# Kernel optimization log

Measured on AMD Instinct MI355X. Metric: run time of the kernel, lower is better.

Reference implementation:

```python
import jax, jax.numpy as jnp
import numpy as np

B, M, K = 32768, 8192, 16
EPS = 1e-5  # torch BatchNorm1d default


def _bn_relu(x, g, b):
    # training-mode batch norm (biased variance), matching torch BatchNorm1d forward
    m = x.mean(0)
    v = x.var(0)
    return jax.nn.relu(g * (x - m) * jax.lax.rsqrt(v + EPS) + b)


def _forward(pos, mc, mv, w1, b1, w2, b2, w3, b3, w4, b4, w5, b5, w6, b6,
             g1, be1, g2, be2, g3, be3, g4, be4, g5, be5, k):
    # squared pairwise distances [B, M]; same ordering as L2 norm used by torch.sort
    d2 = (pos * pos).sum(1, keepdims=True) + (mc * mc).sum(1)[None, :] - 2.0 * (pos @ mc.T)
    _, idx = jax.lax.top_k(-d2, k)                     # k nearest indices [B, k]
    nb = jnp.concatenate([mc[idx], mv[idx]], axis=-1)  # [B, k, 4] = (coord, value) per neighbor
    knn_feat = jnp.concatenate([pos, nb.reshape(pos.shape[0], k * 4)], axis=1)  # [B, 2+4k]
    x = _bn_relu(knn_feat @ w1 + b1, g1, be1)
    x = _bn_relu(x @ w2 + b2, g2, be2)
    x = _bn_relu(x @ w3 + b3, g3, be3)
    x = _bn_relu(x @ w4 + b4, g4, be4)
    x = _bn_relu(x @ w5 + b5, g5, be5)  # dropout = identity (eval mode)
    x = x @ w6 + b6
    return x, knn_feat


def setup_inputs() -> dict:
    key = jax.random.key(0)
    ks = jax.random.split(key, 32)
    d_in = 2 + K * 4
    dims = [(d_in, 128), (128, 256), (256, 512), (512, 128), (128, 64), (64, 2)]
    inp = {
        "pos": jax.random.normal(ks[0], (B, 2), jnp.float32),
        "measure_coords": jax.random.normal(ks[1], (M, 2), jnp.float32),
        "measure_vals": jax.random.normal(ks[2], (M, 2), jnp.float32),
    }
    for i, (fi, fo) in enumerate(dims, 1):
        inp[f"w{i}"] = jax.random.normal(ks[2 + 2 * i], (fi, fo), jnp.float32) / np.float32(np.sqrt(fi))
        inp[f"b{i}"] = jnp.zeros((fo,), jnp.float32)
    for i, n in enumerate([128, 256, 512, 128, 64], 1):
        inp[f"g{i}"] = jnp.ones((n,), jnp.float32)
        inp[f"be{i}"] = jnp.zeros((n,), jnp.float32)
    inp["k"] = K
    return inp


def reference(pos, measure_coords, measure_vals, w1, b1, w2, b2, w3, b3, w4, b4,
              w5, b5, w6, b6, g1, be1, g2, be2, g3, be3, g4, be4, g5, be5, k):
    return _forward(pos, measure_coords, measure_vals, w1, b1, w2, b2, w3, b3, w4,
                    b4, w5, b5, w6, b6, g1, be1, g2, be2, g3, be3, g4, be4, g5, be5, k)
```

## Files before the change

kernel.cpp:

```cpp
#include <hip/hip_runtime.h>

typedef unsigned short u16;
typedef unsigned int   u32;
typedef __attribute__((ext_vector_type(8))) short bf16x8;
typedef __attribute__((ext_vector_type(4))) float f32x4;

#define B_ROWS 32768
#define EPS_BN 1e-5f

__device__ __forceinline__ u16 f2bf(float f) {
  u32 u = __float_as_uint(f);
  u32 r = (u + 0x7FFFu + ((u >> 16) & 1u)) >> 16;
  return (u16)r;
}
__device__ __forceinline__ float bf2f(u16 h) {
  return __uint_as_float(((u32)h) << 16);
}

__device__ __forceinline__ float dcalc(float px, float py, float sp, float mx, float my) {
#pragma clang fp contract(off)
  float sm   = mx * mx + my * my;
  float pm   = px * mx;
  float dot  = __builtin_fmaf(py, my, pm);
  float spsm = sp + sm;
  return spsm - 2.0f * dot;
}
__device__ __forceinline__ float dcalc2(float px, float py, float sp, float mx, float my,
                                        float sm) {
#pragma clang fp contract(off)
  float pm   = px * mx;
  float dot  = __builtin_fmaf(py, my, pm);
  float spsm = sp + sm;
  return spsm - 2.0f * dot;
}
__device__ __forceinline__ float smcalc(float mx, float my) {
#pragma clang fp contract(off)
  return mx * mx + my * my;
}
__device__ __forceinline__ float spcalc(float px, float py) {
#pragma clang fp contract(off)
  return px * px + py * py;
}
#define MED3 __builtin_amdgcn_fmed3f

__global__ __launch_bounds__(256, 4)
void knn_kernel(const float2* __restrict__ pos, const float2* __restrict__ mc,
                const float2* __restrict__ mv, float* __restrict__ knn_out,
                u16* __restrict__ X0)
{
  __shared__ float tv[32 * 130];
  __shared__ float tstS[32];
  __shared__ int   qcnt[32];

  const int t = threadIdx.x;
  const int g = t >> 6;
  const int s = t & 63;
  const int q0 = blockIdx.x * 32;

  float px[8], py[8], sp[8];
#pragma unroll
  for (int j = 0; j < 8; ++j) {
    float2 p = pos[q0 + g * 8 + j];
    px[j] = p.x; py[j] = p.y; sp[j] = spcalc(p.x, p.y);
  }

  const float4* mc4 = (const float4*)mc;
  const int b4 = s * 64;
  const int basePt = s * 128;

  float z0[8], z1[8];
#pragma unroll
  for (int j = 0; j < 8; ++j) { z0[j] = __builtin_inff(); z1[j] = __builtin_inff(); }

  float4 cur = mc4[b4];
  for (int i = 0; i < 64; ++i) {
    float4 nxt = mc4[b4 + ((i + 1) & 63)];
    float smA = smcalc(cur.x, cur.y);
    float smB = smcalc(cur.z, cur.w);
#pragma unroll
    for (int j = 0; j < 8; ++j) {
      float dA = dcalc2(px[j], py[j], sp[j], cur.x, cur.y, smA);
      z1[j] = MED3(z0[j], dA, z1[j]); z0[j] = fminf(z0[j], dA);
      float dB = dcalc2(px[j], py[j], sp[j], cur.z, cur.w, smB);
      z1[j] = MED3(z0[j], dB, z1[j]); z0[j] = fminf(z0[j], dB);
    }
    cur = nxt;
  }
#pragma unroll
  for (int j = 0; j < 8; ++j) {
    tv[(g * 8 + j) * 130 + s * 2 + 0] = z0[j];
    tv[(g * 8 + j) * 130 + s * 2 + 1] = z1[j];
  }
  __syncthreads();

  if (t < 32) {
    float ch[16];
#pragma unroll
    for (int j = 0; j < 16; ++j) ch[j] = __builtin_inff();
    for (int k = 0; k < 128; ++k) {
      float v = tv[t * 130 + k];
#pragma unroll
      for (int j = 15; j >= 1; --j) ch[j] = MED3(ch[j-1], v, ch[j]);
      ch[0] = fminf(ch[0], v);
    }
    tstS[t] = ch[15];
    qcnt[t] = 0;
  }
  __syncthreads();
  float Tq[8];
#pragma unroll
  for (int j = 0; j < 8; ++j) Tq[j] = tstS[g * 8 + j];
  __syncthreads();

  u16* qcand = (u16*)tv;
  for (int i = 0; i < 64; ++i) {
    float4 c2 = mc4[b4 + i];
    float smA = smcalc(c2.x, c2.y);
    float smB = smcalc(c2.z, c2.w);
    const int idxA = basePt + 2 * i;
#pragma unroll
    for (int j = 0; j < 8; ++j) {
      float dA = dcalc2(px[j], py[j], sp[j], c2.x, c2.y, smA);
      if (dA <= Tq[j]) {
        int o = atomicAdd(&qcnt[g * 8 + j], 1);
        if (o < 64) qcand[(g * 8 + j) * 64 + o] = (u16)idxA;
      }
      float dB = dcalc2(px[j], py[j], sp[j], c2.z, c2.w, smB);
      if (dB <= Tq[j]) {
        int o = atomicAdd(&qcnt[g * 8 + j], 1);
        if (o < 64) qcand[(g * 8 + j) * 64 + o] = (u16)(idxA + 1);
      }
    }
  }
  __syncthreads();

  if (t < 32) {
    const int q = q0 + t;
    float2 p = pos[q];
    const float sq = spcalc(p.x, p.y);
    int cnt = qcnt[t]; if (cnt > 64) cnt = 64;
    float fd[16]; int fi[16];
#pragma unroll
    for (int j = 0; j < 16; ++j) { fd[j] = __builtin_inff(); fi[j] = 0x7fffffff; }
    for (int j = 0; j < cnt; ++j) {
      int ci = qcand[t * 64 + j];
      float2 m = mc[ci];
      float d = dcalc(p.x, p.y, sq, m.x, m.y);
      bool cc = (d < fd[15]) || (d == fd[15] && ci < fi[15]);
      if (cc) {
#pragma unroll
        for (int k = 15; k >= 1; --k) {
          bool cm = (d < fd[k-1]) || (d == fd[k-1] && ci < fi[k-1]);
          if (cc) {
            if (cm) { fd[k] = fd[k-1]; fi[k] = fi[k-1]; }
            else    { fd[k] = d;       fi[k] = ci;      }
          }
          cc = cm;
        }
        if (cc) { fd[0] = d; fi[0] = ci; }
      }
    }
    float* orow = knn_out + (size_t)q * 66;
    u16*   xrow = X0 + (size_t)q * 96;
    orow[0] = p.x; orow[1] = p.y;
    xrow[0] = f2bf(p.x); xrow[1] = f2bf(p.y);
#pragma unroll
    for (int j = 0; j < 16; ++j) {
      int ci = fi[j];
      float2 m = mc[ci], v = mv[ci];
      orow[2 + 4*j + 0] = m.x; orow[2 + 4*j + 1] = m.y;
      orow[2 + 4*j + 2] = v.x; orow[2 + 4*j + 3] = v.y;
      xrow[2 + 4*j + 0] = f2bf(m.x); xrow[2 + 4*j + 1] = f2bf(m.y);
      xrow[2 + 4*j + 2] = f2bf(v.x); xrow[2 + 4*j + 3] = f2bf(v.y);
    }
#pragma unroll
    for (int c = 66; c < 96; ++c) xrow[c] = 0;
  }
}

__global__ __launch_bounds__(256)
void prep_wt_all(const float* __restrict__ w1, const float* __restrict__ w2,
                 const float* __restrict__ w3, const float* __restrict__ w4,
                 const float* __restrict__ w5,
                 u16* __restrict__ wt1, u16* __restrict__ wt2, u16* __restrict__ wt3,
                 u16* __restrict__ wt4, u16* __restrict__ wt5)
{
  const int l = blockIdx.y;
  const float* w; u16* wt; int K, N, Kp;
  if (l == 0)      { w = w1; wt = wt1; K = 66;  N = 128; Kp = 96;  }
  else if (l == 1) { w = w2; wt = wt2; K = 128; N = 256; Kp = 128; }
  else if (l == 2) { w = w3; wt = wt3; K = 256; N = 512; Kp = 256; }
  else if (l == 3) { w = w4; wt = wt4; K = 512; N = 128; Kp = 512; }
  else             { w = w5; wt = wt5; K = 128; N = 64;  Kp = 128; }
  int i = blockIdx.x * 256 + threadIdx.x;
  if (i >= N * Kp) return;
  int n = i / Kp, kp = i - n * Kp;
  float v = (kp < K) ? w[(size_t)kp * N + n] : 0.0f;
  wt[i] = f2bf(v);
}

template<int BN, bool FUSE>
__global__ __launch_bounds__(256)
void gemm_bn_kernel(const u16* __restrict__ X, int Kw,
                    const u16* __restrict__ WT,
                    const float* __restrict__ bias,
                    const float* __restrict__ psum, const float* __restrict__ psq,
                    const float* __restrict__ gw,   const float* __restrict__ bw,
                    u16* __restrict__ Z, int N,
                    float* __restrict__ csum, float* __restrict__ csq)
{
  constexpr int BM = 128;
  constexpr int AST = 40;
  __shared__ u16 Ash[BM * AST];
  __shared__ u16 Bsh[BN * AST];
  __shared__ float redS[4][BN];
  __shared__ float redQ[4][BN];
  __shared__ float scA[512];
  __shared__ float ttA[512];

  const int t = threadIdx.x;
  const int wave = t >> 6;
  const int lane = t & 63;
  const int lr = lane & 15;
  const int qd = lane >> 4;
  const int m0 = blockIdx.x * BM;
  const int n0 = blockIdx.y * BN;

  if (FUSE) {
    const float invB = 1.0f / 32768.0f;
    for (int c = t; c < Kw; c += 256) {
      float mean = psum[c] * invB;
      float var  = __fmaf_rn(-mean, mean, psq[c] * invB);
      float sc   = gw[c] * rsqrtf(var + EPS_BN);
      scA[c] = sc;
      ttA[c] = __fmaf_rn(-mean, sc, bw[c]);
    }
    __syncthreads();
  }

  f32x4 acc[2][BN / 16];
#pragma unroll
  for (int a = 0; a < 2; ++a)
#pragma unroll
    for (int b = 0; b < BN / 16; ++b) {
      acc[a][b][0] = 0.f; acc[a][b][1] = 0.f; acc[a][b][2] = 0.f; acc[a][b][3] = 0.f;
    }

  const int sr = t >> 2;
  const int sk = (t & 3) * 8;

  for (int k0 = 0; k0 < Kw; k0 += 32) {
#pragma unroll
    for (int rr = 0; rr < 2; ++rr) {
      int r = sr + rr * 64;
      uint4 g = *(const uint4*)(&X[(size_t)(m0 + r) * Kw + k0 + sk]);
      if (FUSE) {
        u32 w[4] = {g.x, g.y, g.z, g.w};
        u32 o[4];
#pragma unroll
        for (int e = 0; e < 4; ++e) {
          int kk = k0 + sk + 2 * e;
          float lo = bf2f((u16)(w[e] & 0xffffu));
          float hi = bf2f((u16)(w[e] >> 16));
          float yl = fmaxf(__fmaf_rn(lo, scA[kk],     ttA[kk]),     0.0f);
          float yh = fmaxf(__fmaf_rn(hi, scA[kk + 1], ttA[kk + 1]), 0.0f);
          o[e] = (u32)f2bf(yl) | ((u32)f2bf(yh) << 16);
        }
        g.x = o[0]; g.y = o[1]; g.z = o[2]; g.w = o[3];
      }
      *(uint4*)(&Ash[r * AST + sk]) = g;
    }
    if (BN == 128) {
#pragma unroll
      for (int rr = 0; rr < 2; ++rr) {
        int n = sr + rr * 64;
        *(uint4*)(&Bsh[n * AST + sk]) =
            *(const uint4*)(&WT[(size_t)(n0 + n) * Kw + k0 + sk]);
      }
    } else {
      int n = sr;
      *(uint4*)(&Bsh[n * AST + sk]) =
          *(const uint4*)(&WT[(size_t)(n0 + n) * Kw + k0 + sk]);
    }
    __syncthreads();
    bf16x8 af0 = *(const bf16x8*)(&Ash[(wave * 32 + lr) * AST + qd * 8]);
    bf16x8 af1 = *(const bf16x8*)(&Ash[(wave * 32 + 16 + lr) * AST + qd * 8]);
#pragma unroll
    for (int ct = 0; ct < BN / 16; ++ct) {
      bf16x8 bfr = *(const bf16x8*)(&Bsh[(ct * 16 + lr) * AST + qd * 8]);
      acc[0][ct] = __builtin_amdgcn_mfma_f32_16x16x32_bf16(af0, bfr, acc[0][ct], 0, 0, 0);
      acc[1][ct] = __builtin_amdgcn_mfma_f32_16x16x32_bf16(af1, bfr, acc[1][ct], 0, 0, 0);
    }
    __syncthreads();
  }

#pragma unroll
  for (int ct = 0; ct < BN / 16; ++ct) {
    int cg = n0 + ct * 16 + lr;
    float bv = bias[cg];
    float s = 0.f, sqv = 0.f;
#pragma unroll
    for (int rt = 0; rt < 2; ++rt) {
#pragma unroll
      for (int r = 0; r < 4; ++r) {
        float z = acc[rt][ct][r] + bv;
        int row = m0 + wave * 32 + rt * 16 + qd * 4 + r;
        Z[(size_t)row * N + cg] = f2bf(z);
        s += z;
        sqv = __fmaf_rn(z, z, sqv);
      }
    }
    s   += __shfl_xor(s, 16);   s   += __shfl_xor(s, 32);
    sqv += __shfl_xor(sqv, 16); sqv += __shfl_xor(sqv, 32);
    if (qd == 0) { redS[wave][ct * 16 + lr] = s; redQ[wave][ct * 16 + lr] = sqv; }
  }
  __syncthreads();
  if (t < BN) {
    float s  = redS[0][t] + redS[1][t] + redS[2][t] + redS[3][t];
    float sv = redQ[0][t] + redQ[1][t] + redQ[2][t] + redQ[3][t];
    atomicAdd(&csum[n0 + t], s);
    atomicAdd(&csq[n0 + t], sv);
  }
}

__global__ __launch_bounds__(256)
void gemv6_kernel(const u16* __restrict__ Z5, const float* __restrict__ w6,
                  const float* __restrict__ b6,
                  const float* __restrict__ psum, const float* __restrict__ psq,
                  const float* __restrict__ gw,   const float* __restrict__ bw,
                  float* __restrict__ out)
{
  __shared__ float wsh[128];
  __shared__ float scs[64];
  __shared__ float tts[64];
  const int t = threadIdx.x;
  if (t < 128) wsh[t] = w6[t];
  if (t < 64) {
    const float invB = 1.0f / 32768.0f;
    float mean = psum[t] * invB;
    float var  = __fmaf_rn(-mean, mean, psq[t] * invB);
    float sc   = gw[t] * rsqrtf(var + EPS_BN);
    scs[t] = sc;
    tts[t] = __fmaf_rn(-mean, sc, bw[t]);
  }
  __syncthreads();
  const int q = blockIdx.x * 256 + t;
  const uint4* xv = (const uint4*)(Z5 + (size_t)q * 64);
  float a0 = 0.f, a1 = 0.f;
#pragma unroll
  for (int cc = 0; cc < 8; ++cc) {
    uint4 pk = xv[cc];
    u32 u[4] = {pk.x, pk.y, pk.z, pk.w};
#pragma unroll
    for (int uu = 0; uu < 4; ++uu) {
      int k = cc * 8 + uu * 2;
      float z0 = bf2f((u16)(u[uu] & 0xffffu));
      float z1 = bf2f((u16)(u[uu] >> 16));
      float x0 = fmaxf(__fmaf_rn(z0, scs[k],     tts[k]),     0.0f);
      float x1 = fmaxf(__fmaf_rn(z1, scs[k + 1], tts[k + 1]), 0.0f);
      x0 = bf2f(f2bf(x0));
      x1 = bf2f(f2bf(x1));
      a0 = __fmaf_rn(x0, wsh[2 * k + 0], a0);
      a1 = __fmaf_rn(x0, wsh[2 * k + 1], a1);
      a0 = __fmaf_rn(x1, wsh[2 * k + 2], a0);
      a1 = __fmaf_rn(x1, wsh[2 * k + 3], a1);
    }
  }
  float2 o; o.x = a0 + b6[0]; o.y = a1 + b6[1];
  ((float2*)out)[q] = o;
}

extern "C" void kernel_launch(void* const* d_in, const int* in_sizes, int n_in,
                              void* d_out, int out_size, void* d_ws, size_t ws_size,
                              hipStream_t stream)
{
  const float2* pos = (const float2*)d_in[0];
  const float2* mc  = (const float2*)d_in[1];
  const float2* mv  = (const float2*)d_in[2];
  const float* w1 = (const float*)d_in[3];  const float* b1 = (const float*)d_in[4];
  const float* w2 = (const float*)d_in[5];  const float* b2 = (const float*)d_in[6];
  const float* w3 = (const float*)d_in[7];  const float* b3 = (const float*)d_in[8];
  const float* w4 = (const float*)d_in[9];  const float* b4 = (const float*)d_in[10];
  const float* w5 = (const float*)d_in[11]; const float* b5 = (const float*)d_in[12];
  const float* w6 = (const float*)d_in[13]; const float* b6 = (const float*)d_in[14];
  const float* g1 = (const float*)d_in[15]; const float* be1 = (const float*)d_in[16];
  const float* g2 = (const float*)d_in[17]; const float* be2 = (const float*)d_in[18];
  const float* g3 = (const float*)d_in[19]; const float* be3 = (const float*)d_in[20];
  const float* g4 = (const float*)d_in[21]; const float* be4 = (const float*)d_in[22];
  const float* g5 = (const float*)d_in[23]; const float* be5 = (const float*)d_in[24];

  char* ws = (char*)d_ws;
  u16* X0   = (u16*)(ws + 0);
  u16* ZA   = (u16*)(ws + 6291456);
  u16* ZB   = (u16*)(ws + 39845888);
  u16* WT1  = (u16*)(ws + 73400320);
  u16* WT2  = (u16*)(ws + 73424896);
  u16* WT3  = (u16*)(ws + 73490432);
  u16* WT4  = (u16*)(ws + 73752576);
  u16* WT5  = (u16*)(ws + 73883648);
  float* stats = (float*)(ws + 73900032);
  float* s1 = stats;        float* s2 = stats + 128;  float* s3 = stats + 384;
  float* s4 = stats + 896;  float* s5 = stats + 1024;
  float* sqb = stats + 1088;
  float* q1 = sqb;          float* q2 = sqb + 128;    float* q3 = sqb + 384;
  float* q4 = sqb + 896;    float* q5 = sqb + 1024;

  float* outX = (float*)d_out;
  float* outK = outX + 2 * B_ROWS;

  hipMemsetAsync(stats, 0, 2176 * sizeof(float), stream);
  prep_wt_all<<<dim3(512, 5), 256, 0, stream>>>(w1, w2, w3, w4, w5, WT1, WT2, WT3, WT4, WT5);
  knn_kernel<<<dim3(1024), 256, 0, stream>>>(pos, mc, mv, outK, X0);

  gemm_bn_kernel<64, false><<<dim3(256, 2), 256, 0, stream>>>(
      X0, 96, WT1, b1, nullptr, nullptr, nullptr, nullptr, ZA, 128, s1, q1);
  gemm_bn_kernel<64, true><<<dim3(256, 4), 256, 0, stream>>>(
      ZA, 128, WT2, b2, s1, q1, g1, be1, ZB, 256, s2, q2);
  gemm_bn_kernel<64, true><<<dim3(256, 8), 256, 0, stream>>>(
      ZB, 256, WT3, b3, s2, q2, g2, be2, ZA, 512, s3, q3);
  gemm_bn_kernel<64, true><<<dim3(256, 2), 256, 0, stream>>>(
      ZA, 512, WT4, b4, s3, q3, g3, be3, ZB, 128, s4, q4);
  gemm_bn_kernel<64, true><<<dim3(256, 1), 256, 0, stream>>>(
      ZB, 128, WT5, b5, s4, q4, g4, be4, ZA, 64, s5, q5);
  gemv6_kernel<<<dim3(128), 256, 0, stream>>>(ZA, w6, b6, s5, q5, g5, be5, outX);

  (void)in_sizes; (void)n_in; (void)out_size; (void)ws_size;
}
```

Before: 358.6 us.

## Fuse MLP stages into one persistent kernel with software grid barriers

Replaces the weight-prep kernel, the five GEMM+BN launches and the final GEMV with a single persistent kernel of 512 blocks that moves between phases through a sense-reversal grid barrier. The BN+ReLU normalisation is no longer fused into the next GEMM's A-load; it becomes a separate in-place apply pass over each activation buffer. The two wider GEMMs switch to 128-column tiles. This removes launch overhead and the repeated per-tile BN recomputation, but adds extra full read/write passes over the activations and relies on all 512 blocks being co-resident, which is not guaranteed and can deadlock otherwise.

```diff
diff --git a/kernel.cpp b/kernel.cpp
--- a/kernel.cpp
+++ b/kernel.cpp
@@ -178,161 +178,198 @@
   }
 }
 
-__global__ __launch_bounds__(256)
-void prep_wt_all(const float* __restrict__ w1, const float* __restrict__ w2,
-                 const float* __restrict__ w3, const float* __restrict__ w4,
-                 const float* __restrict__ w5,
-                 u16* __restrict__ wt1, u16* __restrict__ wt2, u16* __restrict__ wt3,
-                 u16* __restrict__ wt4, u16* __restrict__ wt5)
-{
-  const int l = blockIdx.y;
-  const float* w; u16* wt; int K, N, Kp;
-  if (l == 0)      { w = w1; wt = wt1; K = 66;  N = 128; Kp = 96;  }
-  else if (l == 1) { w = w2; wt = wt2; K = 128; N = 256; Kp = 128; }
-  else if (l == 2) { w = w3; wt = wt3; K = 256; N = 512; Kp = 256; }
-  else if (l == 3) { w = w4; wt = wt4; K = 512; N = 128; Kp = 512; }
-  else             { w = w5; wt = wt5; K = 128; N = 64;  Kp = 128; }
-  int i = blockIdx.x * 256 + threadIdx.x;
-  if (i >= N * Kp) return;
-  int n = i / Kp, kp = i - n * Kp;
-  float v = (kp < K) ? w[(size_t)kp * N + n] : 0.0f;
-  wt[i] = f2bf(v);
-}
-
-template<int BN, bool FUSE>
-__global__ __launch_bounds__(256)
-void gemm_bn_kernel(const u16* __restrict__ X, int Kw,
-                    const u16* __restrict__ WT,
-                    const float* __restrict__ bias,
-                    const float* __restrict__ psum, const float* __restrict__ psq,
-                    const float* __restrict__ gw,   const float* __restrict__ bw,
-                    u16* __restrict__ Z, int N,
-                    float* __restrict__ csum, float* __restrict__ csq)
-{
-  constexpr int BM = 128;
+struct MlpArgs {
+  const u16* X0;
+  u16 *ZA, *ZB;
+  u16 *WT1, *WT2, *WT3, *WT4, *WT5;
+  const float *w1,*b1,*w2,*b2,*w3,*b3,*w4,*b4,*w5,*b5,*w6,*b6;
+  const float *g1,*be1,*g2,*be2,*g3,*be3,*g4,*be4,*g5,*be5;
+  float* stats;
+  int*   bar;
+  float* outX;
+};
+
+#define MLP_GRID 512
+
+__device__ __forceinline__ void grid_barrier(int* bar, int& sense)
+{
+  __syncthreads();
+  if (threadIdx.x == 0) {
+    ++sense;
+    __threadfence();
+    if (atomicAdd(&bar[0], 1) == MLP_GRID - 1) {
+      atomicExch(&bar[0], 0);
+      __threadfence();
+      atomicExch(&bar[1], sense);
+    } else {
+      while (atomicAdd(&bar[1], 0) < sense) { __builtin_amdgcn_s_sleep(2); }
+    }
+    __threadfence();
+  }
+  __syncthreads();
+}
+
+__device__ void prep_phase(const MlpArgs& a)
+{
+  const int gid  = blockIdx.x * 256 + threadIdx.x;
+  const int nthr = MLP_GRID * 256;
+  if (gid < 2176) a.stats[gid] = 0.0f;
+  for (int i = gid; i < 249856; i += nthr) {
+    int r = i; const float* w; u16* wt; int N, K, Kp;
+    if (r < 12288)                 { w = a.w1; wt = a.WT1; N = 128; K = 66;  Kp = 96;  }
+    else if ((r -= 12288) < 32768) { w = a.w2; wt = a.WT2; N = 256; K = 128; Kp = 128; }
+    else if ((r -= 32768) < 131072){ w = a.w3; wt = a.WT3; N = 512; K = 256; Kp = 256; }
+    else if ((r -= 131072) < 65536){ w = a.w4; wt = a.WT4; N = 128; K = 512; Kp = 512; }
+    else { r -= 65536;               w = a.w5; wt = a.WT5; N = 64;  K = 128; Kp = 128; }
+    int n = r / Kp, kp = r - n * Kp;
+    float v = (kp < K) ? w[(size_t)kp * N + n] : 0.0f;
+    wt[r] = f2bf(v);
+  }
+}
+
+template<int BN>
+__device__ void gemm_phase(const u16* __restrict__ X, int Kw,
+                           const u16* __restrict__ WT, const float* __restrict__ bias,
+                           u16* __restrict__ Z, int N,
+                           float* csum, float* csq, char* smem)
+{
   constexpr int AST = 40;
-  __shared__ u16 Ash[BM * AST];
-  __shared__ u16 Bsh[BN * AST];
-  __shared__ float redS[4][BN];
-  __shared__ float redQ[4][BN];
-  __shared__ float scA[512];
-  __shared__ float ttA[512];
+  u16*   Ash  = (u16*)smem;
+  u16*   Bsh  = (u16*)(smem + 10240);
+  float* redS = (float*)(smem + 20480);
+  float* redQ = (float*)(smem + 22528);
 
   const int t = threadIdx.x;
   const int wave = t >> 6;
   const int lane = t & 63;
   const int lr = lane & 15;
   const int qd = lane >> 4;
-  const int m0 = blockIdx.x * BM;
-  const int n0 = blockIdx.y * BN;
-
-  if (FUSE) {
-    const float invB = 1.0f / 32768.0f;
-    for (int c = t; c < Kw; c += 256) {
-      float mean = psum[c] * invB;
-      float var  = __fmaf_rn(-mean, mean, psq[c] * invB);
-      float sc   = gw[c] * rsqrtf(var + EPS_BN);
-      scA[c] = sc;
-      ttA[c] = __fmaf_rn(-mean, sc, bw[c]);
-    }
-    __syncthreads();
-  }
-
-  f32x4 acc[2][BN / 16];
-#pragma unroll
-  for (int a = 0; a < 2; ++a)
-#pragma unroll
-    for (int b = 0; b < BN / 16; ++b) {
-      acc[a][b][0] = 0.f; acc[a][b][1] = 0.f; acc[a][b][2] = 0.f; acc[a][b][3] = 0.f;
-    }
-
   const int sr = t >> 2;
   const int sk = (t & 3) * 8;
 
-  for (int k0 = 0; k0 < Kw; k0 += 32) {
-#pragma unroll
-    for (int rr = 0; rr < 2; ++rr) {
-      int r = sr + rr * 64;
-      uint4 g = *(const uint4*)(&X[(size_t)(m0 + r) * Kw + k0 + sk]);
-      if (FUSE) {
-        u32 w[4] = {g.x, g.y, g.z, g.w};
-        u32 o[4];
-#pragma unroll
-        for (int e = 0; e < 4; ++e) {
-          int kk = k0 + sk + 2 * e;
-          float lo = bf2f((u16)(w[e] & 0xffffu));
-          float hi = bf2f((u16)(w[e] >> 16));
-          float yl = fmaxf(__fmaf_rn(lo, scA[kk],     ttA[kk]),     0.0f);
-          float yh = fmaxf(__fmaf_rn(hi, scA[kk + 1], ttA[kk + 1]), 0.0f);
-          o[e] = (u32)f2bf(yl) | ((u32)f2bf(yh) << 16);
+  const int nTiles = 256 * (N / BN);
+  for (int tile = blockIdx.x; tile < nTiles; tile += MLP_GRID) {
+    const int m0 = (tile & 255) * 128;
+    const int n0 = (tile >> 8) * BN;
+
+    f32x4 acc[2][BN / 16];
+#pragma unroll
+    for (int aa = 0; aa < 2; ++aa)
+#pragma unroll
+      for (int bb = 0; bb < BN / 16; ++bb) {
+        acc[aa][bb][0] = 0.f; acc[aa][bb][1] = 0.f;
+        acc[aa][bb][2] = 0.f; acc[aa][bb][3] = 0.f;
+      }
+
+    for (int k0 = 0; k0 < Kw; k0 += 32) {
+#pragma unroll
+      for (int rr = 0; rr < 2; ++rr) {
+        int r = sr + rr * 64;
+        *(uint4*)(&Ash[r * AST + sk]) =
+            *(const uint4*)(&X[(size_t)(m0 + r) * Kw + k0 + sk]);
+      }
+      if (BN == 128) {
+#pragma unroll
+        for (int rr = 0; rr < 2; ++rr) {
+          int n = sr + rr * 64;
+          *(uint4*)(&Bsh[n * AST + sk]) =
+              *(const uint4*)(&WT[(size_t)(n0 + n) * Kw + k0 + sk]);
         }
-        g.x = o[0]; g.y = o[1]; g.z = o[2]; g.w = o[3];
-      }
-      *(uint4*)(&Ash[r * AST + sk]) = g;
-    }
-    if (BN == 128) {
-#pragma unroll
-      for (int rr = 0; rr < 2; ++rr) {
-        int n = sr + rr * 64;
+      } else {
+        int n = sr;
         *(uint4*)(&Bsh[n * AST + sk]) =
             *(const uint4*)(&WT[(size_t)(n0 + n) * Kw + k0 + sk]);
       }
-    } else {
-      int n = sr;
-      *(uint4*)(&Bsh[n * AST + sk]) =
-          *(const uint4*)(&WT[(size_t)(n0 + n) * Kw + k0 + sk]);
+      __syncthreads();
+      bf16x8 af0 = *(const bf16x8*)(&Ash[(wave * 32 + lr) * AST + qd * 8]);
+      bf16x8 af1 = *(const bf16x8*)(&Ash[(wave * 32 + 16 + lr) * AST + qd * 8]);
+#pragma unroll
+      for (int ct = 0; ct < BN / 16; ++ct) {
+        bf16x8 bfr = *(const bf16x8*)(&Bsh[(ct * 16 + lr) * AST + qd * 8]);
+        acc[0][ct] = __builtin_amdgcn_mfma_f32_16x16x32_bf16(af0, bfr, acc[0][ct], 0, 0, 0);
+        acc[1][ct] = __builtin_amdgcn_mfma_f32_16x16x32_bf16(af1, bfr, acc[1][ct], 0, 0, 0);
+      }
+      __syncthreads();
+    }
+
+#pragma unroll
+    for (int ct = 0; ct < BN / 16; ++ct) {
+      int cg = n0 + ct * 16 + lr;
+      float bv = bias[cg];
+      float s = 0.f, sqv = 0.f;
+#pragma unroll
+      for (int rt = 0; rt < 2; ++rt) {
+#pragma unroll
+        for (int r = 0; r < 4; ++r) {
+          float z = acc[rt][ct][r] + bv;
+          int row = m0 + wave * 32 + rt * 16 + qd * 4 + r;
+          Z[(size_t)row * N + cg] = f2bf(z);
+          s += z;
+          sqv = __fmaf_rn(z, z, sqv);
+        }
+      }
+      s   += __shfl_xor(s, 16);   s   += __shfl_xor(s, 32);
+      sqv += __shfl_xor(sqv, 16); sqv += __shfl_xor(sqv, 32);
+      if (qd == 0) { redS[wave * BN + ct * 16 + lr] = s; redQ[wave * BN + ct * 16 + lr] = sqv; }
     }
     __syncthreads();
-    bf16x8 af0 = *(const bf16x8*)(&Ash[(wave * 32 + lr) * AST + qd * 8]);
-    bf16x8 af1 = *(const bf16x8*)(&Ash[(wave * 32 + 16 + lr) * AST + qd * 8]);
-#pragma unroll
-    for (int ct = 0; ct < BN / 16; ++ct) {
-      bf16x8 bfr = *(const bf16x8*)(&Bsh[(ct * 16 + lr) * AST + qd * 8]);
-      acc[0][ct] = __builtin_amdgcn_mfma_f32_16x16x32_bf16(af0, bfr, acc[0][ct], 0, 0, 0);
-      acc[1][ct] = __builtin_amdgcn_mfma_f32_16x16x32_bf16(af1, bfr, acc[1][ct], 0, 0, 0);
+    if (t < BN) {
+      float s = 0.f, sv = 0.f;
+#pragma unroll
+      for (int gg = 0; gg < 4; ++gg) { s += redS[gg * BN + t]; sv += redQ[gg * BN + t]; }
+      atomicAdd(&csum[n0 + t], s);
+      atomicAdd(&csq[n0 + t], sv);
     }
     __syncthreads();
   }
-
-#pragma unroll
-  for (int ct = 0; ct < BN / 16; ++ct) {
-    int cg = n0 + ct * 16 + lr;
-    float bv = bias[cg];
-    float s = 0.f, sqv = 0.f;
-#pragma unroll
-    for (int rt = 0; rt < 2; ++rt) {
-#pragma unroll
-      for (int r = 0; r < 4; ++r) {
-        float z = acc[rt][ct][r] + bv;
-        int row = m0 + wave * 32 + rt * 16 + qd * 4 + r;
-        Z[(size_t)row * N + cg] = f2bf(z);
-        s += z;
-        sqv = __fmaf_rn(z, z, sqv);
-      }
-    }
-    s   += __shfl_xor(s, 16);   s   += __shfl_xor(s, 32);
-    sqv += __shfl_xor(sqv, 16); sqv += __shfl_xor(sqv, 32);
-    if (qd == 0) { redS[wave][ct * 16 + lr] = s; redQ[wave][ct * 16 + lr] = sqv; }
-  }
-  __syncthreads();
-  if (t < BN) {
-    float s  = redS[0][t] + redS[1][t] + redS[2][t] + redS[3][t];
-    float sv = redQ[0][t] + redQ[1][t] + redQ[2][t] + redQ[3][t];
-    atomicAdd(&csum[n0 + t], s);
-    atomicAdd(&csq[n0 + t], sv);
-  }
-}
-
-__global__ __launch_bounds__(256)
-void gemv6_kernel(const u16* __restrict__ Z5, const float* __restrict__ w6,
-                  const float* __restrict__ b6,
-                  const float* __restrict__ psum, const float* __restrict__ psq,
-                  const float* __restrict__ gw,   const float* __restrict__ bw,
-                  float* __restrict__ out)
-{
-  __shared__ float wsh[128];
-  __shared__ float scs[64];
-  __shared__ float tts[64];
+}
+
+__device__ void apply_phase(u16* Z, int N, const float* psum, const float* psq,
+                            const float* gw, const float* bw, char* smem)
+{
+  float* sc = (float*)smem;
+  float* tt = (float*)(smem + 2048);
+  const int t = threadIdx.x;
+  const float invB = 1.0f / 32768.0f;
+  for (int c = t; c < N; c += 256) {
+    float mean = psum[c] * invB;
+    float var  = __fmaf_rn(-mean, mean, psq[c] * invB);
+    float s    = gw[c] * rsqrtf(var + EPS_BN);
+    sc[c] = s;
+    tt[c] = __fmaf_rn(-mean, s, bw[c]);
+  }
+  __syncthreads();
+  const int total8 = 32768 * (N / 8);
+  for (int i8 = blockIdx.x * 256 + t; i8 < total8; i8 += MLP_GRID * 256) {
+    uint4 zp = ((const uint4*)Z)[i8];
+    const int c0 = (i8 * 8) & (N - 1);
+    u32 wv[4] = {zp.x, zp.y, zp.z, zp.w};
+    u32 ov[4];
+#pragma unroll
+    for (int u = 0; u < 4; ++u) {
+      u32 res = 0;
+#pragma unroll
+      for (int hl = 0; hl < 2; ++hl) {
+        int c = c0 + 2 * u + hl;
+        float zz = bf2f((u16)((wv[u] >> (16 * hl)) & 0xffffu));
+        float y  = fmaxf(__fmaf_rn(zz, sc[c], tt[c]), 0.0f);
+        res |= ((u32)f2bf(y)) << (16 * hl);
+      }
+      ov[u] = res;
+    }
+    uint4 o4; o4.x = ov[0]; o4.y = ov[1]; o4.z = ov[2]; o4.w = ov[3];
+    ((uint4*)Z)[i8] = o4;
+  }
+  __syncthreads();
+}
+
+__device__ void gemv_phase(const u16* Z5, const float* w6, const float* b6,
+                           const float* psum, const float* psq,
+                           const float* gw, const float* bw, float* out, char* smem)
+{
+  float* wsh = (float*)smem;
+  float* scs = (float*)(smem + 512);
+  float* tts = (float*)(smem + 768);
   const int t = threadIdx.x;
   if (t < 128) wsh[t] = w6[t];
   if (t < 64) {
@@ -344,30 +381,67 @@
     tts[t] = __fmaf_rn(-mean, sc, bw[t]);
   }
   __syncthreads();
-  const int q = blockIdx.x * 256 + t;
-  const uint4* xv = (const uint4*)(Z5 + (size_t)q * 64);
-  float a0 = 0.f, a1 = 0.f;
-#pragma unroll
-  for (int cc = 0; cc < 8; ++cc) {
-    uint4 pk = xv[cc];
-    u32 u[4] = {pk.x, pk.y, pk.z, pk.w};
-#pragma unroll
-    for (int uu = 0; uu < 4; ++uu) {
-      int k = cc * 8 + uu * 2;
-      float z0 = bf2f((u16)(u[uu] & 0xffffu));
-      float z1 = bf2f((u16)(u[uu] >> 16));
-      float x0 = fmaxf(__fmaf_rn(z0, scs[k],     tts[k]),     0.0f);
-      float x1 = fmaxf(__fmaf_rn(z1, scs[k + 1], tts[k + 1]), 0.0f);
-      x0 = bf2f(f2bf(x0));
-      x1 = bf2f(f2bf(x1));
-      a0 = __fmaf_rn(x0, wsh[2 * k + 0], a0);
-      a1 = __fmaf_rn(x0, wsh[2 * k + 1], a1);
-      a0 = __fmaf_rn(x1, wsh[2 * k + 2], a0);
-      a1 = __fmaf_rn(x1, wsh[2 * k + 3], a1);
-    }
-  }
-  float2 o; o.x = a0 + b6[0]; o.y = a1 + b6[1];
-  ((float2*)out)[q] = o;
+  for (int q = blockIdx.x * 256 + t; q < 32768; q += MLP_GRID * 256) {
+    const uint4* xv = (const uint4*)(Z5 + (size_t)q * 64);
+    float a0 = 0.f, a1 = 0.f;
+#pragma unroll
+    for (int cc = 0; cc < 8; ++cc) {
+      uint4 pk = xv[cc];
+      u32 u[4] = {pk.x, pk.y, pk.z, pk.w};
+#pragma unroll
+      for (int uu = 0; uu < 4; ++uu) {
+        int k = cc * 8 + uu * 2;
+        float z0 = bf2f((u16)(u[uu] & 0xffffu));
+        float z1 = bf2f((u16)(u[uu] >> 16));
+        float x0 = fmaxf(__fmaf_rn(z0, scs[k],     tts[k]),     0.0f);
+        float x1 = fmaxf(__fmaf_rn(z1, scs[k + 1], tts[k + 1]), 0.0f);
+        x0 = bf2f(f2bf(x0));
+        x1 = bf2f(f2bf(x1));
+        a0 = __fmaf_rn(x0, wsh[2 * k + 0], a0);
+        a1 = __fmaf_rn(x0, wsh[2 * k + 1], a1);
+        a0 = __fmaf_rn(x1, wsh[2 * k + 2], a0);
+        a1 = __fmaf_rn(x1, wsh[2 * k + 3], a1);
+      }
+    }
+    float2 o; o.x = a0 + b6[0]; o.y = a1 + b6[1];
+    ((float2*)out)[q] = o;
+  }
+}
+
+__global__ __launch_bounds__(256, 2)
+void mlp_kernel(MlpArgs a)
+{
+  __shared__ __align__(16) char smem[24576];
+  int sense = 0;
+  int* bar = a.bar;
+
+  float* s1 = a.stats;        float* s2 = a.stats + 128;  float* s3 = a.stats + 384;
+  float* s4 = a.stats + 896;  float* s5 = a.stats + 1024;
+  float* sqb = a.stats + 1088;
+  float* q1 = sqb;            float* q2 = sqb + 128;      float* q3 = sqb + 384;
+  float* q4 = sqb + 896;      float* q5 = sqb + 1024;
+
+  prep_phase(a);
+  grid_barrier(bar, sense);
+  gemm_phase<64> (a.X0, 96,  a.WT1, a.b1, a.ZA, 128, s1, q1, smem);
+  grid_barrier(bar, sense);
+  apply_phase(a.ZA, 128, s1, q1, a.g1, a.be1, smem);
+  grid_barrier(bar, sense);
+  gemm_phase<128>(a.ZA, 128, a.WT2, a.b2, a.ZB, 256, s2, q2, smem);
+  grid_barrier(bar, sense);
+  apply_phase(a.ZB, 256, s2, q2, a.g2, a.be2, smem);
+  grid_barrier(bar, sense);
+  gemm_phase<128>(a.ZB, 256, a.WT3, a.b3, a.ZA, 512, s3, q3, smem);
+  grid_barrier(bar, sense);
+  apply_phase(a.ZA, 512, s3, q3, a.g3, a.be3, smem);
+  grid_barrier(bar, sense);
+  gemm_phase<64> (a.ZA, 512, a.WT4, a.b4, a.ZB, 128, s4, q4, smem);
+  grid_barrier(bar, sense);
+  apply_phase(a.ZB, 128, s4, q4, a.g4, a.be4, smem);
+  grid_barrier(bar, sense);
+  gemm_phase<64> (a.ZB, 128, a.WT5, a.b5, a.ZA, 64, s5, q5, smem);
+  grid_barrier(bar, sense);
+  gemv_phase(a.ZA, a.w6, a.b6, s5, q5, a.g5, a.be5, a.outX, smem);
 }
 
 extern "C" void kernel_launch(void* const* d_in, const int* in_sizes, int n_in,
@@ -377,17 +451,6 @@
   const float2* pos = (const float2*)d_in[0];
   const float2* mc  = (const float2*)d_in[1];
   const float2* mv  = (const float2*)d_in[2];
-  const float* w1 = (const float*)d_in[3];  const float* b1 = (const float*)d_in[4];
-  const float* w2 = (const float*)d_in[5];  const float* b2 = (const float*)d_in[6];
-  const float* w3 = (const float*)d_in[7];  const float* b3 = (const float*)d_in[8];
-  const float* w4 = (const float*)d_in[9];  const float* b4 = (const float*)d_in[10];
-  const float* w5 = (const float*)d_in[11]; const float* b5 = (const float*)d_in[12];
-  const float* w6 = (const float*)d_in[13]; const float* b6 = (const float*)d_in[14];
-  const float* g1 = (const float*)d_in[15]; const float* be1 = (const float*)d_in[16];
-  const float* g2 = (const float*)d_in[17]; const float* be2 = (const float*)d_in[18];
-  const float* g3 = (const float*)d_in[19]; const float* be3 = (const float*)d_in[20];
-  const float* g4 = (const float*)d_in[21]; const float* be4 = (const float*)d_in[22];
-  const float* g5 = (const float*)d_in[23]; const float* be5 = (const float*)d_in[24];
 
   char* ws = (char*)d_ws;
   u16* X0   = (u16*)(ws + 0);
@@ -399,30 +462,31 @@
   u16* WT4  = (u16*)(ws + 73752576);
   u16* WT5  = (u16*)(ws + 73883648);
   float* stats = (float*)(ws + 73900032);
-  float* s1 = stats;        float* s2 = stats + 128;  float* s3 = stats + 384;
-  float* s4 = stats + 896;  float* s5 = stats + 1024;
-  float* sqb = stats + 1088;
-  float* q1 = sqb;          float* q2 = sqb + 128;    float* q3 = sqb + 384;
-  float* q4 = sqb + 896;    float* q5 = sqb + 1024;
+  int*   bar   = (int*)(ws + 73908736);
 
   float* outX = (float*)d_out;
   float* outK = outX + 2 * B_ROWS;
 
-  hipMemsetAsync(stats, 0, 2176 * sizeof(float), stream);
-  prep_wt_all<<<dim3(512, 5), 256, 0, stream>>>(w1, w2, w3, w4, w5, WT1, WT2, WT3, WT4, WT5);
+  hipMemsetAsync(bar, 0, 2 * sizeof(int), stream);
   knn_kernel<<<dim3(1024), 256, 0, stream>>>(pos, mc, mv, outK, X0);
 
-  gemm_bn_kernel<64, false><<<dim3(256, 2), 256, 0, stream>>>(
-      X0, 96, WT1, b1, nullptr, nullptr, nullptr, nullptr, ZA, 128, s1, q1);
-  gemm_bn_kernel<64, true><<<dim3(256, 4), 256, 0, stream>>>(
-      ZA, 128, WT2, b2, s1, q1, g1, be1, ZB, 256, s2, q2);
-  gemm_bn_kernel<64, true><<<dim3(256, 8), 256, 0, stream>>>(
-      ZB, 256, WT3, b3, s2, q2, g2, be2, ZA, 512, s3, q3);
-  gemm_bn_kernel<64, true><<<dim3(256, 2), 256, 0, stream>>>(
-      ZA, 512, WT4, b4, s3, q3, g3, be3, ZB, 128, s4, q4);
-  gemm_bn_kernel<64, true><<<dim3(256, 1), 256, 0, stream>>>(
-      ZB, 128, WT5, b5, s4, q4, g4, be4, ZA, 64, s5, q5);
-  gemv6_kernel<<<dim3(128), 256, 0, stream>>>(ZA, w6, b6, s5, q5, g5, be5, outX);
+  MlpArgs a;
+  a.X0 = X0; a.ZA = ZA; a.ZB = ZB;
+  a.WT1 = WT1; a.WT2 = WT2; a.WT3 = WT3; a.WT4 = WT4; a.WT5 = WT5;
+  a.w1 = (const float*)d_in[3];  a.b1 = (const float*)d_in[4];
+  a.w2 = (const float*)d_in[5];  a.b2 = (const float*)d_in[6];
+  a.w3 = (const float*)d_in[7];  a.b3 = (const float*)d_in[8];
+  a.w4 = (const float*)d_in[9];  a.b4 = (const float*)d_in[10];
+  a.w5 = (const float*)d_in[11]; a.b5 = (const float*)d_in[12];
+  a.w6 = (const float*)d_in[13]; a.b6 = (const float*)d_in[14];
+  a.g1 = (const float*)d_in[15]; a.be1 = (const float*)d_in[16];
+  a.g2 = (const float*)d_in[17]; a.be2 = (const float*)d_in[18];
+  a.g3 = (const float*)d_in[19]; a.be3 = (const float*)d_in[20];
+  a.g4 = (const float*)d_in[21]; a.be4 = (const float*)d_in[22];
+  a.g5 = (const float*)d_in[23]; a.be5 = (const float*)d_in[24];
+  a.stats = stats; a.bar = bar; a.outX = outX;
+
+  mlp_kernel<<<dim3(MLP_GRID), dim3(256), 0, stream>>>(a);
 
   (void)in_sizes; (void)n_in; (void)out_size; (void)ws_size;
 }
```

Result: slower. 804.0 us (+124.2%).
